# Optimization experiments

Measured on AMD Instinct MI355X. Metric: run time of the kernel, lower is better.

Reference implementation:

```python
import jax, jax.numpy as jnp
import numpy as np

C, K, D = 64, 512, 2048   # classes, shots per class, hidden_dim
N_ITER = 3                # n_routing_iter


def _squash(x):
    # x: (..., d); squash along last axis: x * ||x|| / (1 + ||x||^2)
    n2 = jnp.sum(x * x, axis=-1, keepdims=True)
    n = jnp.sqrt(n2)
    return x * (n / (1.0 + n2))


def setup_inputs() -> dict:
    key = jax.random.key(0)
    z_s = jax.random.normal(key, (C, K, D), dtype=jnp.float32)
    return {"z_s": z_s}


def reference(z_s):
    # z_s: (C, K, D). All C classes routed in parallel (vectorized over the
    # original Python loop over classes).
    z_sq = _squash(z_s)                       # (C, K, D)
    b = jnp.zeros(z_s.shape[:2], z_s.dtype)   # routing logits (C, K)
    c = jnp.zeros((z_s.shape[0], z_s.shape[2]), z_s.dtype)
    for _ in range(N_ITER):
        d = jax.nn.softmax(b, axis=-1)                      # (C, K)
        c = _squash(jnp.einsum('ck,ckd->cd', d, z_sq))      # (C, D)
        b = b + jnp.einsum('ckd,cd->ck', z_sq, c)           # (C, K)
    # returned representative is c from the LAST iteration (b update after is unused,
    # matching the torch loop where c_i from the final iter is appended)
    return c
```

## Files before the change

kernel.cpp:

```cpp
#include <hip/hip_runtime.h>
#include <hip/hip_fp16.h>
#include <math.h>

#define C_CLS   64
#define K_SHOTS 512
#define D_DIM   2048
#define BPC     16
#define ROWS_PER_BLOCK (K_SHOTS / BPC)
#define NWAVES  4
#define ROWS_PER_WAVE (ROWS_PER_BLOCK / NWAVES)
#define NBLK    (C_CLS * BPC)
#define NF4     8
#define NH4     4

__device__ __forceinline__ uint2 pack4(float4 v) {
    union { uint2 u; __half2 h[2]; } pk;
    pk.h[0] = __floats2half2_rn(v.x, v.y);
    pk.h[1] = __floats2half2_rn(v.z, v.w);
    return pk.u;
}

__device__ __forceinline__ float wave_reduce_sum(float v) {
#pragma unroll
    for (int off = 32; off > 0; off >>= 1)
        v += __shfl_xor(v, off, 64);
    return v;
}

__global__ __launch_bounds__(256)
void route_pass0(const float* __restrict__ z,
                 __half* __restrict__ z16,
                 __half* __restrict__ part_s,
                 float* __restrict__ part_e)
{
    __shared__ float4 s_comb[NWAVES][D_DIM / 4];
    __shared__ float  e_comb[NWAVES];

    const int blk  = blockIdx.x;
    const int cls  = blk >> 4;
    const int bic  = blk & (BPC - 1);
    const int lane = threadIdx.x & 63;
    const int wid  = threadIdx.x >> 6;
    const int t    = threadIdx.x;

    float4 acc[NF4];
#pragma unroll
    for (int i = 0; i < NF4; ++i) acc[i] = make_float4(0.f, 0.f, 0.f, 0.f);
    float esum = 0.f;

    const int k0 = bic * ROWS_PER_BLOCK + wid * ROWS_PER_WAVE;
    const float4* __restrict__ zb =
        (const float4*)(z + ((size_t)cls * K_SHOTS + k0) * D_DIM);

    float4 zcur[NF4];
#pragma unroll
    for (int i = 0; i < NF4; ++i) zcur[i] = zb[lane + i * 64];

#pragma unroll
    for (int r = 0; r < ROWS_PER_WAVE; ++r) {
        float4 znext[NF4];
        if (r + 1 < ROWS_PER_WAVE) {
            const float4* zn = zb + (size_t)(r + 1) * (D_DIM / 4);
#pragma unroll
            for (int i = 0; i < NF4; ++i) znext[i] = zn[lane + i * 64];
        }
        float n2 = 0.f;
#pragma unroll
        for (int i = 0; i < NF4; ++i)
            n2 += zcur[i].x * zcur[i].x + zcur[i].y * zcur[i].y
                + zcur[i].z * zcur[i].z + zcur[i].w * zcur[i].w;
        n2 = wave_reduce_sum(n2);
        const float sc = sqrtf(n2) / (1.f + n2);

        uint2* p16 = (uint2*)(z16 + ((size_t)cls * K_SHOTS + k0 + r) * D_DIM);
#pragma unroll
        for (int i = 0; i < NF4; ++i) {
            float4 s;
            s.x = sc * zcur[i].x; s.y = sc * zcur[i].y;
            s.z = sc * zcur[i].z; s.w = sc * zcur[i].w;
            p16[lane + i * 64] = pack4(s);
            acc[i].x += s.x; acc[i].y += s.y; acc[i].z += s.z; acc[i].w += s.w;
        }
        esum += 1.f;

        if (r + 1 < ROWS_PER_WAVE) {
#pragma unroll
            for (int i = 0; i < NF4; ++i) zcur[i] = znext[i];
        }
    }

#pragma unroll
    for (int i = 0; i < NF4; ++i) s_comb[wid][lane + i * 64] = acc[i];
    if (lane == 0) e_comb[wid] = esum;
    __syncthreads();

    uint2* ps = (uint2*)(part_s + (size_t)blk * D_DIM);
#pragma unroll
    for (int j = 0; j < 2; ++j) {
        const int f = t + j * 256;
        const float4 a  = s_comb[0][f];
        const float4 b4 = s_comb[1][f];
        const float4 c4 = s_comb[2][f];
        const float4 d4 = s_comb[3][f];
        float4 s;
        s.x = (a.x + b4.x) + (c4.x + d4.x);
        s.y = (a.y + b4.y) + (c4.y + d4.y);
        s.z = (a.z + b4.z) + (c4.z + d4.z);
        s.w = (a.w + b4.w) + (c4.w + d4.w);
        ps[f] = pack4(s);
    }
    if (t == 0) part_e[blk] = (e_comb[0] + e_comb[1]) + (e_comb[2] + e_comb[3]);
}

template <int PASS>
__global__ __launch_bounds__(256)
void route_pass_h(const __half* __restrict__ z16,
                  float* __restrict__ bvec,
                  const float* __restrict__ c_prev,
                  __half* __restrict__ part_s,
                  float* __restrict__ part_e)
{
    __shared__ float4 s_comb[NWAVES][D_DIM / 4];
    __shared__ float  e_comb[NWAVES];

    const int rawblk = blockIdx.x;
    const int blk  = (PASS == 1) ? (NBLK - 1 - rawblk) : rawblk;
    const int cls  = blk >> 4;
    const int bic  = blk & (BPC - 1);
    const int lane = threadIdx.x & 63;
    const int wid  = threadIdx.x >> 6;
    const int t    = threadIdx.x;

    const float4* cp4 = (const float4*)(c_prev + (size_t)cls * D_DIM);
    float4 cpA[NH4], cpB[NH4];
#pragma unroll
    for (int j = 0; j < NH4; ++j) {
        const int c2i = 2 * (lane + j * 64);
        cpA[j] = cp4[c2i];
        cpB[j] = cp4[c2i + 1];
    }

    float4 acc[2 * NH4];
#pragma unroll
    for (int i = 0; i < 2 * NH4; ++i) acc[i] = make_float4(0.f, 0.f, 0.f, 0.f);
    float esum = 0.f;

    const int k0 = bic * ROWS_PER_BLOCK + wid * ROWS_PER_WAVE;
    const float4* __restrict__ zb =
        (const float4*)(z16 + ((size_t)cls * K_SHOTS + k0) * D_DIM);

    const int r0    = (PASS == 1) ? (ROWS_PER_WAVE - 1) : 0;
    const int rstep = (PASS == 1) ? -1 : 1;

    float4 zcur[NH4];
#pragma unroll
    for (int j = 0; j < NH4; ++j)
        zcur[j] = zb[(size_t)r0 * (D_DIM / 8) + lane + j * 64];

#pragma unroll
    for (int rr = 0; rr < ROWS_PER_WAVE; ++rr) {
        const int r = r0 + rr * rstep;
        float4 znext[NH4];
        if (rr + 1 < ROWS_PER_WAVE) {
            const float4* zn = zb + (size_t)(r + rstep) * (D_DIM / 8);
#pragma unroll
            for (int j = 0; j < NH4; ++j) znext[j] = zn[lane + j * 64];
        }

        float dot = 0.f;
#pragma unroll
        for (int j = 0; j < NH4; ++j) {
            const __half2* hp = (const __half2*)&zcur[j];
            const float2 a0 = __half22float2(hp[0]);
            const float2 a1 = __half22float2(hp[1]);
            const float2 a2 = __half22float2(hp[2]);
            const float2 a3 = __half22float2(hp[3]);
            dot += a0.x * cpA[j].x + a0.y * cpA[j].y
                 + a1.x * cpA[j].z + a1.y * cpA[j].w
                 + a2.x * cpB[j].x + a2.y * cpB[j].y
                 + a3.x * cpB[j].z + a3.y * cpB[j].w;
        }
        dot = wave_reduce_sum(dot);

        const int k = k0 + r;
        float bnew = dot;
        if (PASS == 2) bnew += bvec[cls * K_SHOTS + k];
        if (PASS == 1 && lane == 0) bvec[cls * K_SHOTS + k] = bnew;
        const float w = expf(bnew);
        esum += w;

#pragma unroll
        for (int j = 0; j < NH4; ++j) {
            const __half2* hp = (const __half2*)&zcur[j];
            const float2 a0 = __half22float2(hp[0]);
            const float2 a1 = __half22float2(hp[1]);
            const float2 a2 = __half22float2(hp[2]);
            const float2 a3 = __half22float2(hp[3]);
            acc[2 * j].x     += w * a0.x;  acc[2 * j].y     += w * a0.y;
            acc[2 * j].z     += w * a1.x;  acc[2 * j].w     += w * a1.y;
            acc[2 * j + 1].x += w * a2.x;  acc[2 * j + 1].y += w * a2.y;
            acc[2 * j + 1].z += w * a3.x;  acc[2 * j + 1].w += w * a3.y;
        }

        if (rr + 1 < ROWS_PER_WAVE) {
#pragma unroll
            for (int j = 0; j < NH4; ++j) zcur[j] = znext[j];
        }
    }

#pragma unroll
    for (int j = 0; j < NH4; ++j) {
        const int c2i = 2 * (lane + j * 64);
        s_comb[wid][c2i]     = acc[2 * j];
        s_comb[wid][c2i + 1] = acc[2 * j + 1];
    }
    if (lane == 0) e_comb[wid] = esum;
    __syncthreads();

    uint2* ps = (uint2*)(part_s + (size_t)blk * D_DIM);
#pragma unroll
    for (int j = 0; j < 2; ++j) {
        const int f = t + j * 256;
        const float4 a  = s_comb[0][f];
        const float4 b4 = s_comb[1][f];
        const float4 c4 = s_comb[2][f];
        const float4 d4 = s_comb[3][f];
        float4 s;
        s.x = (a.x + b4.x) + (c4.x + d4.x);
        s.y = (a.y + b4.y) + (c4.y + d4.y);
        s.z = (a.z + b4.z) + (c4.z + d4.z);
        s.w = (a.w + b4.w) + (c4.w + d4.w);
        ps[f] = pack4(s);
    }
    if (t == 0) part_e[blk] = (e_comb[0] + e_comb[1]) + (e_comb[2] + e_comb[3]);
}

__global__ __launch_bounds__(256)
void reduce_squash(const __half* __restrict__ part_s,
                   const float* __restrict__ part_e,
                   float* __restrict__ c_out)
{
    __shared__ float wred[NWAVES];
    const int cls  = blockIdx.x;
    const int t    = threadIdx.x;
    const int lane = t & 63;
    const int wid  = t >> 6;

    float esum = 0.f;
#pragma unroll
    for (int p = 0; p < BPC; ++p) esum += part_e[cls * BPC + p];
    const float inv = 1.f / esum;

    float4 m[2];
    float n2p = 0.f;
#pragma unroll
    for (int j = 0; j < 2; ++j) {
        const int f = t + j * 256;
        float4 s = make_float4(0.f, 0.f, 0.f, 0.f);
#pragma unroll
        for (int p = 0; p < BPC; ++p) {
            const uint2 v =
                ((const uint2*)(part_s + (size_t)(cls * BPC + p) * D_DIM))[f];
            const __half2* hv = (const __half2*)&v;
            const float2 lo = __half22float2(hv[0]);
            const float2 hi = __half22float2(hv[1]);
            s.x += lo.x; s.y += lo.y; s.z += hi.x; s.w += hi.y;
        }
        m[j].x = s.x * inv; m[j].y = s.y * inv;
        m[j].z = s.z * inv; m[j].w = s.w * inv;
        n2p += m[j].x * m[j].x + m[j].y * m[j].y
             + m[j].z * m[j].z + m[j].w * m[j].w;
    }
    float n2 = wave_reduce_sum(n2p);
    if (lane == 0) wred[wid] = n2;
    __syncthreads();
    n2 = (wred[0] + wred[1]) + (wred[2] + wred[3]);
    const float fac = sqrtf(n2) / (1.f + n2);

    float4* co = (float4*)(c_out + (size_t)cls * D_DIM);
#pragma unroll
    for (int j = 0; j < 2; ++j) {
        const int f = t + j * 256;
        float4 o;
        o.x = m[j].x * fac; o.y = m[j].y * fac;
        o.z = m[j].z * fac; o.w = m[j].w * fac;
        co[f] = o;
    }
}

extern "C" void kernel_launch(void* const* d_in, const int* in_sizes, int n_in,
                              void* d_out, int out_size, void* d_ws, size_t ws_size,
                              hipStream_t stream)
{
    const float* z = (const float*)d_in[0];
    float* out = (float*)d_out;
    float* ws  = (float*)d_ws;

    float*  bvec   = ws;
    float*  part_e = bvec + C_CLS * K_SHOTS;
    float*  c_buf  = part_e + NBLK;
    __half* part_s = (__half*)(c_buf + (size_t)C_CLS * D_DIM);
    __half* z16    = part_s + (size_t)NBLK * D_DIM;

    route_pass0<<<NBLK, 256, 0, stream>>>(z, z16, part_s, part_e);
    reduce_squash<<<C_CLS, 256, 0, stream>>>(part_s, part_e, c_buf);

    route_pass_h<1><<<NBLK, 256, 0, stream>>>(z16, bvec, c_buf, part_s, part_e);
    reduce_squash<<<C_CLS, 256, 0, stream>>>(part_s, part_e, c_buf);

    route_pass_h<2><<<NBLK, 256, 0, stream>>>(z16, bvec, c_buf, part_s, part_e);
    reduce_squash<<<C_CLS, 256, 0, stream>>>(part_s, part_e, out);
}
```

Baseline: 155.8 us.

## Fuse routing passes into one cooperative kernel with grid syncs

Replaces the six kernel launches with one cooperative persistent kernel of 512 blocks that separates the routing stages with grid-wide barriers. It keeps the first-pass logits in registers instead of a global b vector and prefetches the fp16 rows before each class reduction. The aim is to remove launch gaps and the round trip of b through memory. In exchange it adds grid-sync overhead, halves the number of blocks that do the bandwidth work, and has only 64 blocks active during each reduction stage; the old multi-kernel path is kept as a fallback.

```diff
diff --git a/kernel.cpp b/kernel.cpp
--- a/kernel.cpp
+++ b/kernel.cpp
@@ -1,17 +1,26 @@
 #include <hip/hip_runtime.h>
+#include <hip/hip_cooperative_groups.h>
 #include <hip/hip_fp16.h>
 #include <math.h>
 
 #define C_CLS   64
 #define K_SHOTS 512
 #define D_DIM   2048
-#define BPC     16
-#define ROWS_PER_BLOCK (K_SHOTS / BPC)
 #define NWAVES  4
-#define ROWS_PER_WAVE (ROWS_PER_BLOCK / NWAVES)
-#define NBLK    (C_CLS * BPC)
 #define NF4     8
 #define NH4     4
+
+#define BPC_C   8
+#define RPB_C   (K_SHOTS / BPC_C)
+#define RPW_C   (RPB_C / NWAVES)
+#define NBLK_C  (C_CLS * BPC_C)
+
+#define BPC_F   16
+#define RPB_F   (K_SHOTS / BPC_F)
+#define RPW_F   (RPB_F / NWAVES)
+#define NBLK_F  (C_CLS * BPC_F)
+
+namespace cg = cooperative_groups;
 
 __device__ __forceinline__ uint2 pack4(float4 v) {
     union { uint2 u; __half2 h[2]; } pk;
@@ -26,6 +35,349 @@
         v += __shfl_xor(v, off, 64);
     return v;
 }
+
+__device__ __forceinline__ void gsync(cg::grid_group& g) {
+    __threadfence();
+    g.sync();
+    __threadfence();
+}
+
+
+__device__ __forceinline__ void class_reduce_c(const __half* __restrict__ ps_cls,
+                                               float inv,
+                                               float* __restrict__ dst,
+                                               int t, int lane, int wid,
+                                               float* e_red)
+{
+    float4 m[2];
+    float n2p = 0.f;
+#pragma unroll
+    for (int j = 0; j < 2; ++j) {
+        const int f = t + j * 256;
+        float4 s = make_float4(0.f, 0.f, 0.f, 0.f);
+#pragma unroll
+        for (int p = 0; p < BPC_C; ++p) {
+            const uint2 v = ((const uint2*)(ps_cls + (size_t)p * D_DIM))[f];
+            const __half2* hv = (const __half2*)&v;
+            const float2 lo = __half22float2(hv[0]);
+            const float2 hi = __half22float2(hv[1]);
+            s.x += lo.x; s.y += lo.y; s.z += hi.x; s.w += hi.y;
+        }
+        m[j].x = s.x * inv; m[j].y = s.y * inv;
+        m[j].z = s.z * inv; m[j].w = s.w * inv;
+        n2p += m[j].x * m[j].x + m[j].y * m[j].y
+             + m[j].z * m[j].z + m[j].w * m[j].w;
+    }
+    float n2 = wave_reduce_sum(n2p);
+    if (lane == 0) e_red[wid] = n2;
+    __syncthreads();
+    n2 = (e_red[0] + e_red[1]) + (e_red[2] + e_red[3]);
+    const float fac = sqrtf(n2) / (1.f + n2);
+    float4* co = (float4*)dst;
+#pragma unroll
+    for (int j = 0; j < 2; ++j) {
+        const int f = t + j * 256;
+        float4 o;
+        o.x = m[j].x * fac; o.y = m[j].y * fac;
+        o.z = m[j].z * fac; o.w = m[j].w * fac;
+        co[f] = o;
+    }
+    __syncthreads();
+}
+
+__global__ __launch_bounds__(256, 2)
+void induction_fused(const float* __restrict__ z,
+                     __half* __restrict__ z16,
+                     __half* __restrict__ part_s,
+                     float* __restrict__ part_e,
+                     float* __restrict__ c_buf,
+                     float* __restrict__ out)
+{
+    cg::grid_group grid = cg::this_grid();
+
+    __shared__ float4 s_comb[NWAVES][D_DIM / 4];
+    __shared__ float  e_comb[NWAVES];
+
+    const int blk  = blockIdx.x;
+    const int cls  = blk >> 3;
+    const int bic  = blk & (BPC_C - 1);
+    const int lane = threadIdx.x & 63;
+    const int wid  = threadIdx.x >> 6;
+    const int t    = threadIdx.x;
+    const int k0   = bic * RPB_C + wid * RPW_C;
+
+    {
+        float4 acc[NF4];
+#pragma unroll
+        for (int i = 0; i < NF4; ++i) acc[i] = make_float4(0.f, 0.f, 0.f, 0.f);
+
+        const float4* __restrict__ zb =
+            (const float4*)(z + ((size_t)cls * K_SHOTS + k0) * D_DIM);
+
+        float4 zcur[NF4];
+#pragma unroll
+        for (int i = 0; i < NF4; ++i) zcur[i] = zb[lane + i * 64];
+
+#pragma unroll
+        for (int r = 0; r < RPW_C; ++r) {
+            float4 znext[NF4];
+            if (r + 1 < RPW_C) {
+                const float4* zn = zb + (size_t)(r + 1) * (D_DIM / 4);
+#pragma unroll
+                for (int i = 0; i < NF4; ++i) znext[i] = zn[lane + i * 64];
+            }
+            float n2 = 0.f;
+#pragma unroll
+            for (int i = 0; i < NF4; ++i)
+                n2 += zcur[i].x * zcur[i].x + zcur[i].y * zcur[i].y
+                    + zcur[i].z * zcur[i].z + zcur[i].w * zcur[i].w;
+            n2 = wave_reduce_sum(n2);
+            const float sc = sqrtf(n2) / (1.f + n2);
+
+            uint2* p16 = (uint2*)(z16 + ((size_t)cls * K_SHOTS + k0 + r) * D_DIM);
+#pragma unroll
+            for (int i = 0; i < NF4; ++i) {
+                float4 s;
+                s.x = sc * zcur[i].x; s.y = sc * zcur[i].y;
+                s.z = sc * zcur[i].z; s.w = sc * zcur[i].w;
+                p16[lane + i * 64] = pack4(s);
+                acc[i].x += s.x; acc[i].y += s.y; acc[i].z += s.z; acc[i].w += s.w;
+            }
+            if (r + 1 < RPW_C) {
+#pragma unroll
+                for (int i = 0; i < NF4; ++i) zcur[i] = znext[i];
+            }
+        }
+
+#pragma unroll
+        for (int i = 0; i < NF4; ++i) s_comb[wid][lane + i * 64] = acc[i];
+        __syncthreads();
+        uint2* ps = (uint2*)(part_s + (size_t)blk * D_DIM);
+#pragma unroll
+        for (int j = 0; j < 2; ++j) {
+            const int f = t + j * 256;
+            const float4 a  = s_comb[0][f];
+            const float4 b4 = s_comb[1][f];
+            const float4 c4 = s_comb[2][f];
+            const float4 d4 = s_comb[3][f];
+            float4 s;
+            s.x = (a.x + b4.x) + (c4.x + d4.x);
+            s.y = (a.y + b4.y) + (c4.y + d4.y);
+            s.z = (a.z + b4.z) + (c4.z + d4.z);
+            s.w = (a.w + b4.w) + (c4.w + d4.w);
+            ps[f] = pack4(s);
+        }
+    }
+
+    gsync(grid);
+
+    const float4* __restrict__ zh =
+        (const float4*)(z16 + ((size_t)cls * K_SHOTS + k0) * D_DIM);
+
+    float4 hcur[NH4];
+#pragma unroll
+    for (int j = 0; j < NH4; ++j) hcur[j] = zh[lane + j * 64];
+
+    if (blk < C_CLS)
+        class_reduce_c(part_s + (size_t)blk * BPC_C * D_DIM, 1.f / (float)K_SHOTS,
+                       c_buf + (size_t)blk * D_DIM, t, lane, wid, e_comb);
+
+    gsync(grid);
+
+    float b1reg[RPW_C];
+    float esum;
+
+    {
+        const float4* cp4 = (const float4*)(c_buf + (size_t)cls * D_DIM);
+        float4 cpA[NH4], cpB[NH4];
+#pragma unroll
+        for (int j = 0; j < NH4; ++j) {
+            const int c2i = 2 * (lane + j * 64);
+            cpA[j] = cp4[c2i];
+            cpB[j] = cp4[c2i + 1];
+        }
+        float4 acc[2 * NH4];
+#pragma unroll
+        for (int i = 0; i < 2 * NH4; ++i) acc[i] = make_float4(0.f, 0.f, 0.f, 0.f);
+        esum = 0.f;
+
+#pragma unroll
+        for (int rr = 0; rr < RPW_C; ++rr) {
+            float4 znext[NH4];
+            if (rr + 1 < RPW_C) {
+                const float4* zn = zh + (size_t)(rr + 1) * (D_DIM / 8);
+#pragma unroll
+                for (int j = 0; j < NH4; ++j) znext[j] = zn[lane + j * 64];
+            }
+            float dot = 0.f;
+#pragma unroll
+            for (int j = 0; j < NH4; ++j) {
+                const __half2* hp = (const __half2*)&hcur[j];
+                const float2 a0 = __half22float2(hp[0]);
+                const float2 a1 = __half22float2(hp[1]);
+                const float2 a2 = __half22float2(hp[2]);
+                const float2 a3 = __half22float2(hp[3]);
+                dot += a0.x * cpA[j].x + a0.y * cpA[j].y
+                     + a1.x * cpA[j].z + a1.y * cpA[j].w
+                     + a2.x * cpB[j].x + a2.y * cpB[j].y
+                     + a3.x * cpB[j].z + a3.y * cpB[j].w;
+            }
+            dot = wave_reduce_sum(dot);
+            b1reg[rr] = dot;
+            const float w = expf(dot);
+            esum += w;
+#pragma unroll
+            for (int j = 0; j < NH4; ++j) {
+                const __half2* hp = (const __half2*)&hcur[j];
+                const float2 a0 = __half22float2(hp[0]);
+                const float2 a1 = __half22float2(hp[1]);
+                const float2 a2 = __half22float2(hp[2]);
+                const float2 a3 = __half22float2(hp[3]);
+                acc[2 * j].x     += w * a0.x;  acc[2 * j].y     += w * a0.y;
+                acc[2 * j].z     += w * a1.x;  acc[2 * j].w     += w * a1.y;
+                acc[2 * j + 1].x += w * a2.x;  acc[2 * j + 1].y += w * a2.y;
+                acc[2 * j + 1].z += w * a3.x;  acc[2 * j + 1].w += w * a3.y;
+            }
+            if (rr + 1 < RPW_C) {
+#pragma unroll
+                for (int j = 0; j < NH4; ++j) hcur[j] = znext[j];
+            }
+        }
+
+#pragma unroll
+        for (int j = 0; j < NH4; ++j) {
+            const int c2i = 2 * (lane + j * 64);
+            s_comb[wid][c2i]     = acc[2 * j];
+            s_comb[wid][c2i + 1] = acc[2 * j + 1];
+        }
+        if (lane == 0) e_comb[wid] = esum;
+        __syncthreads();
+        uint2* ps = (uint2*)(part_s + (size_t)blk * D_DIM);
+#pragma unroll
+        for (int j = 0; j < 2; ++j) {
+            const int f = t + j * 256;
+            const float4 a  = s_comb[0][f];
+            const float4 b4 = s_comb[1][f];
+            const float4 c4 = s_comb[2][f];
+            const float4 d4 = s_comb[3][f];
+            float4 s;
+            s.x = (a.x + b4.x) + (c4.x + d4.x);
+            s.y = (a.y + b4.y) + (c4.y + d4.y);
+            s.z = (a.z + b4.z) + (c4.z + d4.z);
+            s.w = (a.w + b4.w) + (c4.w + d4.w);
+            ps[f] = pack4(s);
+        }
+        if (t == 0) part_e[blk] = (e_comb[0] + e_comb[1]) + (e_comb[2] + e_comb[3]);
+    }
+
+    gsync(grid);
+
+#pragma unroll
+    for (int j = 0; j < NH4; ++j) hcur[j] = zh[lane + j * 64];
+
+    if (blk < C_CLS) {
+        float es = 0.f;
+#pragma unroll
+        for (int p = 0; p < BPC_C; ++p) es += part_e[blk * BPC_C + p];
+        class_reduce_c(part_s + (size_t)blk * BPC_C * D_DIM, 1.f / es,
+                       c_buf + (size_t)blk * D_DIM, t, lane, wid, e_comb);
+    }
+
+    gsync(grid);
+
+    {
+        const float4* cp4 = (const float4*)(c_buf + (size_t)cls * D_DIM);
+        float4 cpA[NH4], cpB[NH4];
+#pragma unroll
+        for (int j = 0; j < NH4; ++j) {
+            const int c2i = 2 * (lane + j * 64);
+            cpA[j] = cp4[c2i];
+            cpB[j] = cp4[c2i + 1];
+        }
+        float4 acc[2 * NH4];
+#pragma unroll
+        for (int i = 0; i < 2 * NH4; ++i) acc[i] = make_float4(0.f, 0.f, 0.f, 0.f);
+        esum = 0.f;
+
+#pragma unroll
+        for (int rr = 0; rr < RPW_C; ++rr) {
+            float4 znext[NH4];
+            if (rr + 1 < RPW_C) {
+                const float4* zn = zh + (size_t)(rr + 1) * (D_DIM / 8);
+#pragma unroll
+                for (int j = 0; j < NH4; ++j) znext[j] = zn[lane + j * 64];
+            }
+            float dot = 0.f;
+#pragma unroll
+            for (int j = 0; j < NH4; ++j) {
+                const __half2* hp = (const __half2*)&hcur[j];
+                const float2 a0 = __half22float2(hp[0]);
+                const float2 a1 = __half22float2(hp[1]);
+                const float2 a2 = __half22float2(hp[2]);
+                const float2 a3 = __half22float2(hp[3]);
+                dot += a0.x * cpA[j].x + a0.y * cpA[j].y
+                     + a1.x * cpA[j].z + a1.y * cpA[j].w
+                     + a2.x * cpB[j].x + a2.y * cpB[j].y
+                     + a3.x * cpB[j].z + a3.y * cpB[j].w;
+            }
+            dot = wave_reduce_sum(dot);
+            const float w = expf(b1reg[rr] + dot);
+            esum += w;
+#pragma unroll
+            for (int j = 0; j < NH4; ++j) {
+                const __half2* hp = (const __half2*)&hcur[j];
+                const float2 a0 = __half22float2(hp[0]);
+                const float2 a1 = __half22float2(hp[1]);
+                const float2 a2 = __half22float2(hp[2]);
+                const float2 a3 = __half22float2(hp[3]);
+                acc[2 * j].x     += w * a0.x;  acc[2 * j].y     += w * a0.y;
+                acc[2 * j].z     += w * a1.x;  acc[2 * j].w     += w * a1.y;
+                acc[2 * j + 1].x += w * a2.x;  acc[2 * j + 1].y += w * a2.y;
+                acc[2 * j + 1].z += w * a3.x;  acc[2 * j + 1].w += w * a3.y;
+            }
+            if (rr + 1 < RPW_C) {
+#pragma unroll
+                for (int j = 0; j < NH4; ++j) hcur[j] = znext[j];
+            }
+        }
+
+#pragma unroll
+        for (int j = 0; j < NH4; ++j) {
+            const int c2i = 2 * (lane + j * 64);
+            s_comb[wid][c2i]     = acc[2 * j];
+            s_comb[wid][c2i + 1] = acc[2 * j + 1];
+        }
+        if (lane == 0) e_comb[wid] = esum;
+        __syncthreads();
+        uint2* ps = (uint2*)(part_s + (size_t)blk * D_DIM);
+#pragma unroll
+        for (int j = 0; j < 2; ++j) {
+            const int f = t + j * 256;
+            const float4 a  = s_comb[0][f];
+            const float4 b4 = s_comb[1][f];
+            const float4 c4 = s_comb[2][f];
+            const float4 d4 = s_comb[3][f];
+            float4 s;
+            s.x = (a.x + b4.x) + (c4.x + d4.x);
+            s.y = (a.y + b4.y) + (c4.y + d4.y);
+            s.z = (a.z + b4.z) + (c4.z + d4.z);
+            s.w = (a.w + b4.w) + (c4.w + d4.w);
+            ps[f] = pack4(s);
+        }
+        if (t == 0) part_e[blk] = (e_comb[0] + e_comb[1]) + (e_comb[2] + e_comb[3]);
+    }
+
+    gsync(grid);
+
+    if (blk < C_CLS) {
+        float es = 0.f;
+#pragma unroll
+        for (int p = 0; p < BPC_C; ++p) es += part_e[blk * BPC_C + p];
+        class_reduce_c(part_s + (size_t)blk * BPC_C * D_DIM, 1.f / es,
+                       out + (size_t)blk * D_DIM, t, lane, wid, e_comb);
+    }
+}
+
 
 __global__ __launch_bounds__(256)
 void route_pass0(const float* __restrict__ z,
@@ -38,7 +390,7 @@
 
     const int blk  = blockIdx.x;
     const int cls  = blk >> 4;
-    const int bic  = blk & (BPC - 1);
+    const int bic  = blk & (BPC_F - 1);
     const int lane = threadIdx.x & 63;
     const int wid  = threadIdx.x >> 6;
     const int t    = threadIdx.x;
@@ -48,7 +400,7 @@
     for (int i = 0; i < NF4; ++i) acc[i] = make_float4(0.f, 0.f, 0.f, 0.f);
     float esum = 0.f;
 
-    const int k0 = bic * ROWS_PER_BLOCK + wid * ROWS_PER_WAVE;
+    const int k0 = bic * RPB_F + wid * RPW_F;
     const float4* __restrict__ zb =
         (const float4*)(z + ((size_t)cls * K_SHOTS + k0) * D_DIM);
 
@@ -57,9 +409,9 @@
     for (int i = 0; i < NF4; ++i) zcur[i] = zb[lane + i * 64];
 
 #pragma unroll
-    for (int r = 0; r < ROWS_PER_WAVE; ++r) {
+    for (int r = 0; r < RPW_F; ++r) {
         float4 znext[NF4];
-        if (r + 1 < ROWS_PER_WAVE) {
+        if (r + 1 < RPW_F) {
             const float4* zn = zb + (size_t)(r + 1) * (D_DIM / 4);
 #pragma unroll
             for (int i = 0; i < NF4; ++i) znext[i] = zn[lane + i * 64];
@@ -82,8 +434,7 @@
             acc[i].x += s.x; acc[i].y += s.y; acc[i].z += s.z; acc[i].w += s.w;
         }
         esum += 1.f;
-
-        if (r + 1 < ROWS_PER_WAVE) {
+        if (r + 1 < RPW_F) {
 #pragma unroll
             for (int i = 0; i < NF4; ++i) zcur[i] = znext[i];
         }
@@ -124,9 +475,9 @@
     __shared__ float  e_comb[NWAVES];
 
     const int rawblk = blockIdx.x;
-    const int blk  = (PASS == 1) ? (NBLK - 1 - rawblk) : rawblk;
+    const int blk  = (PASS == 1) ? (NBLK_F - 1 - rawblk) : rawblk;
     const int cls  = blk >> 4;
-    const int bic  = blk & (BPC - 1);
+    const int bic  = blk & (BPC_F - 1);
     const int lane = threadIdx.x & 63;
     const int wid  = threadIdx.x >> 6;
     const int t    = threadIdx.x;
@@ -145,11 +496,11 @@
     for (int i = 0; i < 2 * NH4; ++i) acc[i] = make_float4(0.f, 0.f, 0.f, 0.f);
     float esum = 0.f;
 
-    const int k0 = bic * ROWS_PER_BLOCK + wid * ROWS_PER_WAVE;
+    const int k0 = bic * RPB_F + wid * RPW_F;
     const float4* __restrict__ zb =
         (const float4*)(z16 + ((size_t)cls * K_SHOTS + k0) * D_DIM);
 
-    const int r0    = (PASS == 1) ? (ROWS_PER_WAVE - 1) : 0;
+    const int r0    = (PASS == 1) ? (RPW_F - 1) : 0;
     const int rstep = (PASS == 1) ? -1 : 1;
 
     float4 zcur[NH4];
@@ -158,10 +509,10 @@
         zcur[j] = zb[(size_t)r0 * (D_DIM / 8) + lane + j * 64];
 
 #pragma unroll
-    for (int rr = 0; rr < ROWS_PER_WAVE; ++rr) {
+    for (int rr = 0; rr < RPW_F; ++rr) {
         const int r = r0 + rr * rstep;
         float4 znext[NH4];
-        if (rr + 1 < ROWS_PER_WAVE) {
+        if (rr + 1 < RPW_F) {
             const float4* zn = zb + (size_t)(r + rstep) * (D_DIM / 8);
 #pragma unroll
             for (int j = 0; j < NH4; ++j) znext[j] = zn[lane + j * 64];
@@ -202,7 +553,7 @@
             acc[2 * j + 1].z += w * a3.x;  acc[2 * j + 1].w += w * a3.y;
         }
 
-        if (rr + 1 < ROWS_PER_WAVE) {
+        if (rr + 1 < RPW_F) {
 #pragma unroll
             for (int j = 0; j < NH4; ++j) zcur[j] = znext[j];
         }
@@ -248,7 +599,7 @@
 
     float esum = 0.f;
 #pragma unroll
-    for (int p = 0; p < BPC; ++p) esum += part_e[cls * BPC + p];
+    for (int p = 0; p < BPC_F; ++p) esum += part_e[cls * BPC_F + p];
     const float inv = 1.f / esum;
 
     float4 m[2];
@@ -258,9 +609,9 @@
         const int f = t + j * 256;
         float4 s = make_float4(0.f, 0.f, 0.f, 0.f);
 #pragma unroll
-        for (int p = 0; p < BPC; ++p) {
+        for (int p = 0; p < BPC_F; ++p) {
             const uint2 v =
-                ((const uint2*)(part_s + (size_t)(cls * BPC + p) * D_DIM))[f];
+                ((const uint2*)(part_s + (size_t)(cls * BPC_F + p) * D_DIM))[f];
             const __half2* hv = (const __half2*)&v;
             const float2 lo = __half22float2(hv[0]);
             const float2 hi = __half22float2(hv[1]);
@@ -293,21 +644,37 @@
                               hipStream_t stream)
 {
     const float* z = (const float*)d_in[0];
-    float* out = (float*)d_out;
-    float* ws  = (float*)d_ws;
+    float* outp = (float*)d_out;
+    float* ws   = (float*)d_ws;
 
     float*  bvec   = ws;
     float*  part_e = bvec + C_CLS * K_SHOTS;
-    float*  c_buf  = part_e + NBLK;
+    float*  c_buf  = part_e + NBLK_F;
     __half* part_s = (__half*)(c_buf + (size_t)C_CLS * D_DIM);
-    __half* z16    = part_s + (size_t)NBLK * D_DIM;
-
-    route_pass0<<<NBLK, 256, 0, stream>>>(z, z16, part_s, part_e);
-    reduce_squash<<<C_CLS, 256, 0, stream>>>(part_s, part_e, c_buf);
-
-    route_pass_h<1><<<NBLK, 256, 0, stream>>>(z16, bvec, c_buf, part_s, part_e);
-    reduce_squash<<<C_CLS, 256, 0, stream>>>(part_s, part_e, c_buf);
-
-    route_pass_h<2><<<NBLK, 256, 0, stream>>>(z16, bvec, c_buf, part_s, part_e);
-    reduce_squash<<<C_CLS, 256, 0, stream>>>(part_s, part_e, out);
-}
+    __half* z16    = part_s + (size_t)NBLK_F * D_DIM;
+
+    int occ = 0;
+    hipError_t qerr = hipOccupancyMaxActiveBlocksPerMultiprocessor(
+        &occ, (const void*)induction_fused, 256, 0);
+    hipError_t lerr = hipErrorUnknown;
+    if (qerr == hipSuccess && occ >= 2) {
+        void* args[6];
+        args[0] = (void*)&z;
+        args[1] = (void*)&z16;
+        args[2] = (void*)&part_s;
+        args[3] = (void*)&part_e;
+        args[4] = (void*)&c_buf;
+        args[5] = (void*)&outp;
+        lerr = hipLaunchCooperativeKernel((const void*)induction_fused,
+                                          dim3(NBLK_C), dim3(256), args, 0, stream);
+    }
+    if (lerr != hipSuccess) {
+        (void)hipGetLastError();
+        route_pass0<<<NBLK_F, 256, 0, stream>>>(z, z16, part_s, part_e);
+        reduce_squash<<<C_CLS, 256, 0, stream>>>(part_s, part_e, c_buf);
+        route_pass_h<1><<<NBLK_F, 256, 0, stream>>>(z16, bvec, c_buf, part_s, part_e);
+        reduce_squash<<<C_CLS, 256, 0, stream>>>(part_s, part_e, c_buf);
+        route_pass_h<2><<<NBLK_F, 256, 0, stream>>>(z16, bvec, c_buf, part_s, part_e);
+        reduce_squash<<<C_CLS, 256, 0, stream>>>(part_s, part_e, outp);
+    }
+}
```

New measurement: 155.1 us. No clear change (-0.4%).
